# Kernel optimization log

Hardware: AMD Instinct MI355X
Metric: run time of the kernel (lower is better)

## Reference

```python
import jax, jax.numpy as jnp
import numpy as np

B, S, D = 2, 2048, 1024
NH, NKV = 16, 4
HD = D // NH
KVD = NKV * HD
NE, MM = 8, 4
INTER = MM * D // NE  # 512
ROPE_BASE = 10000.0
ALPHA, BETA, GATE, DT = 0.95, 0.3, 0.1, 0.1
MU_MIN, MU_MAX, VMAX = 0.5, 1.5, 3.0


def rms_norm(x):
    # torch F.rms_norm with eps=None -> finfo(dtype).eps, no learned weight
    return x * jax.lax.rsqrt(jnp.mean(x * x, axis=-1, keepdims=True) + jnp.finfo(x.dtype).eps)


def rope_tables(seq_len, dtype):
    inv_freq = 1.0 / ROPE_BASE ** (jnp.arange(0, HD, 2, dtype=jnp.float32) / HD)
    t = jnp.arange(seq_len, dtype=jnp.float32)
    freqs = jnp.outer(t, inv_freq)  # [S, HD/2]
    return jnp.cos(freqs).astype(dtype)[None, None], jnp.sin(freqs).astype(dtype)[None, None]


def apply_rotary(x, cos, sin):
    half = x.shape[-1] // 2
    x1, x2 = x[..., :half], x[..., half:]
    return jnp.concatenate((x1 * cos + x2 * sin, -x1 * sin + x2 * cos), axis=-1)


def attention(n, cq_w, ck_w, cv_w, proj_w, q_gain):
    q = jnp.einsum('bsd,od->bso', n, cq_w).reshape(B, S, NH, HD).transpose(0, 2, 1, 3)
    k = jnp.einsum('bsd,od->bso', n, ck_w).reshape(B, S, NKV, HD).transpose(0, 2, 1, 3)
    v = jnp.einsum('bsd,od->bso', n, cv_w).reshape(B, S, NKV, HD).transpose(0, 2, 1, 3)
    q, k = rms_norm(q), rms_norm(k)
    cos, sin = rope_tables(S, q.dtype)
    q, k = apply_rotary(q, cos, sin), apply_rotary(k, cos, sin)
    q = q * q_gain[None, :, None, None]
    rep = NH // NKV  # GQA: repeat kv heads
    k = jnp.repeat(k, rep, axis=1)
    v = jnp.repeat(v, rep, axis=1)
    scale = 1.0 / np.sqrt(HD).astype(np.float32)
    scores = jnp.einsum('bhqd,bhkd->bhqk', q, k) * scale
    causal = jnp.tril(jnp.ones((S, S), bool))
    scores = jnp.where(causal[None, None], scores, jnp.finfo(scores.dtype).min)
    probs = jax.nn.softmax(scores, axis=-1)
    y = jnp.einsum('bhqk,bhkd->bhqd', probs, v)
    y = y.transpose(0, 2, 1, 3).reshape(B, S, D)
    return jnp.einsum('bsd,od->bso', y, proj_w)


def moe(m, gate_up, down, eids):
    # faithful to TokenRoutedMLP: dense per-expert GEMM, masked accumulate
    flat = m.reshape(-1, D)
    fids = eids.reshape(-1)
    out = jnp.zeros_like(flat)
    for e in range(NE):
        gu = flat @ gate_up[e]                       # [T, 2*INTER]
        g, u = gu[:, :INTER], gu[:, INTER:]
        h = (jax.nn.silu(g) * u) @ down[e]           # [T, D]
        out = out + h * (fids == e)[:, None].astype(flat.dtype)
    return out.reshape(B, S, D)


def setup_inputs():
    key = jax.random.key(0)
    ks = jax.random.split(key, 10)
    w = lambda k, shape: jax.random.normal(k, shape, jnp.float32) * 0.02
    return {
        'x': jax.random.normal(ks[0], (B, S, D), jnp.float32),
        'x0': jax.random.normal(ks[1], (B, S, D), jnp.float32),
        'vel': jnp.zeros((B, S, D), jnp.float32),
        'resid_mix': jnp.stack((jnp.ones(D, jnp.float32), jnp.zeros(D, jnp.float32))),
        'attn_scale': jnp.ones(D, jnp.float32),
        'mlp_scale': jnp.ones(D, jnp.float32),
        'cq_w': w(ks[2], (D, D)),
        'ck_w': w(ks[3], (KVD, D)),
        'cv_w': w(ks[4], (KVD, D)),
        'proj_w': w(ks[5], (D, D)),
        'q_gain': jnp.ones(NH, jnp.float32),
        'mu': jnp.full((D,), 1.0, jnp.float32),
        'gate_up': w(ks[6], (NE, D, 2 * INTER)),
        'down': w(ks[7], (NE, INTER, D)),
        'eids': jax.random.randint(ks[8], (B, S), 0, NE),
    }


def reference(x, x0, vel, resid_mix, attn_scale, mlp_scale, cq_w, ck_w, cv_w, proj_w, q_gain, mu, gate_up, down, eids):
    x = resid_mix[0][None, None, :] * x + resid_mix[1][None, None, :] * x0
    n = rms_norm(x)
    x = x + attn_scale[None, None, :] * attention(n, cq_w, ck_w, cv_w, proj_w, q_gain)
    # PID dynamics
    mu_c = jnp.clip(mu, MU_MIN, MU_MAX)
    v_next = jnp.clip(ALPHA * vel - BETA * (x - mu_c[None, None, :]), -VMAX, VMAX)
    x = x + DT * GATE * v_next
    x = x + mlp_scale[None, None, :] * moe(rms_norm(x), gate_up, down, eids)
    return x, v_next
```

## Files before the change

### kernel.cpp

```cpp
#include <hip/hip_runtime.h>
#include <hip/hip_bf16.h>
#include <math.h>

#define NBATCH 2
#define NSEQ   2048
#define NDIM   1024
#define NHEAD  16
#define NKVH   4
#define HDIM   64
#define KVD    256
#define NEXP   8
#define NINTER 512
#define NTOK   (NBATCH*NSEQ)
#define QKVN   1536
#define MAXTILE 40
#define RMS_EPS 1.1920929e-07f
#define LN_10000 9.210340371976184f
#define QSCALE (0.125f * 1.44269504088896f)
#define DEFER_THR 11.5f
#define LOG2E 1.44269504088896f

typedef __attribute__((ext_vector_type(8))) short bf16x8;
typedef __attribute__((ext_vector_type(4))) short short4v;
typedef __attribute__((ext_vector_type(4))) float f32x4;

__device__ __forceinline__ short f2b(float f) {
  return __builtin_bit_cast(short, (__bf16)f);
}
__device__ __forceinline__ float b2f(short s) {
  unsigned u = ((unsigned)(unsigned short)s) << 16;
  return __builtin_bit_cast(float, u);
}
__device__ __forceinline__ float ex2(float x) {
  float r; asm("v_exp_f32 %0, %1" : "=v"(r) : "v"(x)); return r;
}
__device__ __forceinline__ void load_lds16(const short* g, short* l) {
  __builtin_amdgcn_global_load_lds((const __attribute__((address_space(1))) void*)g,
                                   (__attribute__((address_space(3))) void*)l, 16, 0, 0);
}

__device__ __forceinline__ float wred64(float v) {
#pragma unroll
  for (int m = 32; m >= 1; m >>= 1) v += __shfl_xor(v, m);
  return v;
}

__global__ __launch_bounds__(256) void k_w_prep(
    const float* __restrict__ cq, const float* __restrict__ ck,
    const float* __restrict__ cv, const float* __restrict__ pw,
    const float* __restrict__ gate_up,
    short* __restrict__ wqkv, short* __restrict__ wproj, short* __restrict__ wgu_t) {
  __shared__ short T[64*66];
  const int bid = blockIdx.x;
  const int t = threadIdx.x;
  if (bid < 2560) {
    const int row = bid;
    const int c = t * 4;
    const float* src; short* dst;
    if (row < 1024)      { src = cq + (size_t)row*NDIM;        dst = wqkv + (size_t)row*NDIM; }
    else if (row < 1280) { src = ck + (size_t)(row-1024)*NDIM; dst = wqkv + (size_t)row*NDIM; }
    else if (row < 1536) { src = cv + (size_t)(row-1280)*NDIM; dst = wqkv + (size_t)row*NDIM; }
    else                 { src = pw + (size_t)(row-1536)*NDIM; dst = wproj + (size_t)(row-1536)*NDIM; }
    float4 v = *(const float4*)(src + c);
    short4v o = {f2b(v.x), f2b(v.y), f2b(v.z), f2b(v.w)};
    *(short4v*)(dst + c) = o;
  } else {
    const int b2 = bid - 2560;
    const int kt = b2 & 15, nt = (b2 >> 4) & 15, e = b2 >> 8;
    const float* ie = gate_up + (size_t)e*1024*1024 + (size_t)(kt*64)*1024 + nt*64;
    short* we = wgu_t + (size_t)e*1024*1024;
    const int r = t >> 4, c = (t & 15) * 4;
#pragma unroll
    for (int p = 0; p < 4; ++p) {
      float4 v = *(const float4*)(ie + (size_t)(p*16 + r)*1024 + c);
      T[(p*16 + r)*66 + c + 0] = f2b(v.x);
      T[(p*16 + r)*66 + c + 1] = f2b(v.y);
      T[(p*16 + r)*66 + c + 2] = f2b(v.z);
      T[(p*16 + r)*66 + c + 3] = f2b(v.w);
    }
    __syncthreads();
#pragma unroll
    for (int p = 0; p < 4; ++p) {
      int rr = p*16 + r;
      int R = nt*64 + rr;
      int Rn = (R < 512) ? ((R & ~15)*2 + (R & 15))
                         : (((R - 512) & ~15)*2 + 16 + (R & 15));
      short4v o = {T[(c+0)*66 + rr], T[(c+1)*66 + rr], T[(c+2)*66 + rr], T[(c+3)*66 + rr]};
      *(short4v*)(we + (size_t)Rn*1024 + kt*64 + c) = o;
    }
  }
}

__global__ __launch_bounds__(256) void k_w_transpose(
    const float* __restrict__ in, short* __restrict__ outp, int KIN, int NIN) {
  __shared__ short T[64*66];
  const int kt = blockIdx.x, nt = blockIdx.y, e = blockIdx.z;
  const float* ie = in + (size_t)e*KIN*NIN + (size_t)(kt*64)*NIN + nt*64;
  short* oe = outp + (size_t)e*NIN*KIN + (size_t)(nt*64)*KIN + kt*64;
  const int t = threadIdx.x;
  const int r = t >> 4, c = (t & 15) * 4;
#pragma unroll
  for (int p = 0; p < 4; ++p) {
    float4 v = *(const float4*)(ie + (size_t)(p*16 + r)*NIN + c);
    T[(p*16 + r)*66 + c + 0] = f2b(v.x);
    T[(p*16 + r)*66 + c + 1] = f2b(v.y);
    T[(p*16 + r)*66 + c + 2] = f2b(v.z);
    T[(p*16 + r)*66 + c + 3] = f2b(v.w);
  }
  __syncthreads();
#pragma unroll
  for (int p = 0; p < 4; ++p) {
    int rr = p*16 + r;
    short4v o = {T[(c+0)*66 + rr], T[(c+1)*66 + rr], T[(c+2)*66 + rr], T[(c+3)*66 + rr]};
    *(short4v*)(oe + (size_t)rr*KIN + c) = o;
  }
}

__global__ __launch_bounds__(256) void k_resid_rms(
    const float* __restrict__ x, const float* __restrict__ x0,
    const float* __restrict__ rmix, short* __restrict__ xr, short* __restrict__ nrm) {
  const int row = blockIdx.x;
  const int t = threadIdx.x;
  const int d = t * 4;
  const size_t base = (size_t)row * NDIM + d;
  float4 a  = *(const float4*)(x  + base);
  float4 b  = *(const float4*)(x0 + base);
  float4 m0 = *(const float4*)(rmix + d);
  float4 m1 = *(const float4*)(rmix + NDIM + d);
  float4 r;
  r.x = m0.x*a.x + m1.x*b.x;
  r.y = m0.y*a.y + m1.y*b.y;
  r.z = m0.z*a.z + m1.z*b.z;
  r.w = m0.w*a.w + m1.w*b.w;
  float ss = r.x*r.x + r.y*r.y + r.z*r.z + r.w*r.w;
  ss = wred64(ss);
  __shared__ float wsum[4];
  if ((t & 63) == 0) wsum[t >> 6] = ss;
  __syncthreads();
  float tot = wsum[0] + wsum[1] + wsum[2] + wsum[3];
  float rms = rsqrtf(tot * (1.0f/NDIM) + RMS_EPS);
  short4v xo = {f2b(r.x), f2b(r.y), f2b(r.z), f2b(r.w)};
  short4v no = {f2b(r.x*rms), f2b(r.y*rms), f2b(r.z*rms), f2b(r.w*rms)};
  *(short4v*)(xr + base) = xo;
  *(short4v*)(nrm + base) = no;
}

template <int MODE>
__global__ __launch_bounds__(256) void k_gemm_mfma(
    const short* __restrict__ A, int lda,
    const short* __restrict__ Bw, int K, int N,
    short* __restrict__ Cb, float* __restrict__ Cf, int ldc,
    const int* __restrict__ rowmap, const int* __restrict__ tiletab,
    const int* __restrict__ meta, const float* __restrict__ mscale) {
  __shared__ short sA[2][128*32];
  __shared__ short sB[2][128*32];
  int row0, end = 0x7fffffff, e = 0;
  if (MODE == 0) {
    row0 = blockIdx.y * 128;
  } else {
    e = tiletab[2*blockIdx.y];
    if (e < 0) return;
    row0 = tiletab[2*blockIdx.y + 1];
    end = meta[1 + e];
  }
  const int t = threadIdx.x;
  const int w = t >> 6, l = t & 63;
  const int wr = (w >> 1) * 64, wc = (w & 1) * 64;
  const int lrow = l & 15, lk8 = (l >> 4) * 8;
  const int srow0 = w*16 + (l >> 2);
  const int scol = (l & 3) * 8;
  const short* Bp = Bw + (size_t)e * N * K + (size_t)(blockIdx.x * 128) * K;
  const short* gA0;
  const short* gA1;
  if (MODE == 1 || MODE == 3) {
    int s0 = row0 + srow0;      if (s0 >= NTOK) s0 = NTOK - 1;
    int s1 = row0 + 64 + srow0; if (s1 >= NTOK) s1 = NTOK - 1;
    gA0 = A + (size_t)rowmap[s0] * lda + scol;
    gA1 = A + (size_t)rowmap[s1] * lda + scol;
  } else {
    gA0 = A + (size_t)(row0 + srow0) * lda + scol;
    gA1 = A + (size_t)(row0 + 64 + srow0) * lda + scol;
  }
  const short* gB0 = Bp + (size_t)srow0 * K + scol;
  const short* gB1 = Bp + (size_t)(64 + srow0) * K + scol;
  const int lo0 = (w*16)*32;
  const int lo1 = (64 + w*16)*32;
  f32x4 acc[4][4];
#pragma unroll
  for (int m = 0; m < 4; ++m)
#pragma unroll
    for (int n = 0; n < 4; ++n) acc[m][n] = 0.f;
  load_lds16(gA0, sA[0] + lo0);
  load_lds16(gA1, sA[0] + lo1);
  load_lds16(gB0, sB[0] + lo0);
  load_lds16(gB1, sB[0] + lo1);
  gA0 += 32; gA1 += 32; gB0 += 32; gB1 += 32;
  int cur = 0;
  for (int k0 = 0; k0 < K; k0 += 32) {
    __syncthreads();
    if (k0 + 32 < K) {
      load_lds16(gA0, sA[cur^1] + lo0);
      load_lds16(gA1, sA[cur^1] + lo1);
      load_lds16(gB0, sB[cur^1] + lo0);
      load_lds16(gB1, sB[cur^1] + lo1);
      gA0 += 32; gA1 += 32; gB0 += 32; gB1 += 32;
    }
    bf16x8 af[4], bfr[4];
#pragma unroll
    for (int m = 0; m < 4; ++m)
      af[m] = *(const bf16x8*)&sA[cur][(wr + m*16 + lrow)*32 + lk8];
#pragma unroll
    for (int n = 0; n < 4; ++n)
      bfr[n] = *(const bf16x8*)&sB[cur][(wc + n*16 + lrow)*32 + lk8];
    __builtin_amdgcn_s_setprio(1);
#pragma unroll
    for (int m = 0; m < 4; ++m)
#pragma unroll
      for (int n = 0; n < 4; ++n)
        acc[m][n] = __builtin_amdgcn_mfma_f32_16x16x32_bf16(af[m], bfr[n], acc[m][n], 0, 0, 0);
    __builtin_amdgcn_s_setprio(0);
    cur ^= 1;
  }
  const int col0 = blockIdx.x * 128;
  if (MODE <= 1) {
#pragma unroll
    for (int m = 0; m < 4; ++m) {
#pragma unroll
      for (int r = 0; r < 4; ++r) {
        int rr = row0 + wr + m*16 + (l >> 4)*4 + r;
        if (rr < end) {
#pragma unroll
          for (int n = 0; n < 4; ++n)
            Cb[(size_t)rr * ldc + col0 + wc + n*16 + lrow] = f2b(acc[m][n][r]);
        }
      }
    }
  } else if (MODE == 2) {
#pragma unroll
    for (int m = 0; m < 4; ++m) {
#pragma unroll
      for (int r = 0; r < 4; ++r) {
        int slot = row0 + wr + m*16 + (l >> 4)*4 + r;
        if (slot < end) {
          int tok = rowmap[slot];
#pragma unroll
          for (int n = 0; n < 4; ++n) {
            int cc = col0 + wc + n*16 + lrow;
            Cf[(size_t)tok * ldc + cc] += mscale[cc] * acc[m][n][r];
          }
        }
      }
    }
  } else {
    const int fbBase = (col0 + wc) >> 5;
#pragma unroll
    for (int m = 0; m < 4; ++m) {
#pragma unroll
      for (int r = 0; r < 4; ++r) {
        int slot = row0 + wr + m*16 + (l >> 4)*4 + r;
        if (slot < end) {
#pragma unroll
          for (int p = 0; p < 2; ++p) {
            float gg = acc[m][2*p][r], uu = acc[m][2*p+1][r];
            float sg = 1.0f / (1.0f + ex2(-LOG2E * gg));
            Cb[(size_t)slot * NINTER + (fbBase + p)*16 + lrow] = f2b(gg * sg * uu);
          }
        }
      }
    }
  }
}

__global__ __launch_bounds__(256) void k_qk_norm_rope(
    short* __restrict__ qkv, const float* __restrict__ q_gain, short* __restrict__ vbT) {
  __shared__ short T[64*72];
  const int row = blockIdx.x;
  const int t = threadIdx.x;
  const int w = t >> 6, lane = t & 63;
  const int s = row & (NSEQ - 1);
  const int fi = lane & 31;
  const float fr = (float)s * expf(-(float)fi * (LN_10000 / 32.0f));
  const float co = cosf(fr), si = sinf(fr);
#pragma unroll
  for (int h = w; h < NHEAD; h += 4) {
    short* p = qkv + (size_t)row*QKVN + h*HDIM + lane;
    float v = b2f(*p);
    float ssum = wred64(v*v);
    float rr = rsqrtf(ssum * (1.0f/HDIM) + RMS_EPS);
    float vn = v * rr;
    float partner = __shfl_xor(vn, 32);
    float o = (lane < 32) ? (vn*co + partner*si) : (vn*co - partner*si);
    *p = f2b(o * q_gain[h] * QSCALE);
  }
  if (w < NKVH) {
    short* p = qkv + (size_t)row*QKVN + 1024 + w*HDIM + lane;
    float v = b2f(*p);
    float ssum = wred64(v*v);
    float rr = rsqrtf(ssum * (1.0f/HDIM) + RMS_EPS);
    float vn = v * rr;
    float partner = __shfl_xor(vn, 32);
    float o = (lane < 32) ? (vn*co + partner*si) : (vn*co - partner*si);
    *p = f2b(o);
  }
  if (row < 256) {
    const int st = row & 31, kh = (row >> 5) & 3, b = row >> 7;
#pragma unroll
    for (int i = 0; i < 2; ++i) {
      int c = t + i*256;
      int sV = c >> 3, d0 = (c & 7) * 8;
      bf16x8 v = *(const bf16x8*)(qkv + (size_t)(b*NSEQ + st*64 + sV)*QKVN + 1280 + kh*HDIM + d0);
#pragma unroll
      for (int j = 0; j < 8; ++j) T[(d0 + j)*72 + sV] = v[j];
    }
    __syncthreads();
#pragma unroll
    for (int i = 0; i < 2; ++i) {
      int c = t + i*256;
      int d = c >> 3, s0 = (c & 7) * 8;
      *(bf16x8*)(vbT + (size_t)((b*NKVH + kh)*HDIM + d)*NSEQ + st*64 + s0) = *(bf16x8*)&T[d*72 + s0];
    }
  }
}

__global__ __launch_bounds__(256) void k_attn_mfma(
    const short* __restrict__ qkv, const short* __restrict__ vbT, short* __restrict__ y) {
  __shared__ short Ks[2][64*72];
  __shared__ short Vt[2][64*72];
  __shared__ short Ps[64*72];
  const int t = threadIdx.x;
  const int l = t & 63, w = t >> 6;
  const int lrow = l & 15, g = l >> 4, lk8 = g * 8;
  const int bid = blockIdx.x;
  int qt = bid & 15;
  const int h = (bid >> 4) & 15, b = bid >> 8;
  if (b & 1) qt = 15 - qt;
  const int kh = h >> 2;
  bf16x8 qf[2][2];
#pragma unroll
  for (int qra = 0; qra < 2; ++qra) {
    int qrow_g = b*NSEQ + qt*128 + qra*64 + w*16 + lrow;
#pragma unroll
    for (int hf = 0; hf < 2; ++hf)
      qf[qra][hf] = *(const bf16x8*)(qkv + (size_t)qrow_g*QKVN + h*HDIM + hf*32 + lk8);
  }
  const int r0a = t >> 3;
  const int d0a = (t & 7) * 8;
  const short* kgbase = qkv + 1024 + (size_t)kh*HDIM;
  const short* vgbase = vbT + (size_t)((b*NKVH + kh)*HDIM)*NSEQ;
  bf16x8 kr0, kr1, vr0, vr1;
#define LOADKV(KT) do { \
    kr0 = *(const bf16x8*)(kgbase + (size_t)(b*NSEQ + (KT)*64 + r0a)*QKVN + d0a); \
    kr1 = *(const bf16x8*)(kgbase + (size_t)(b*NSEQ + (KT)*64 + r0a + 32)*QKVN + d0a); \
    vr0 = *(const bf16x8*)(vgbase + (size_t)r0a*NSEQ + (KT)*64 + d0a); \
    vr1 = *(const bf16x8*)(vgbase + (size_t)(r0a + 32)*NSEQ + (KT)*64 + d0a); \
  } while (0)
  float m_i[2] = {-INFINITY, -INFINITY};
  float l_i[2] = {0.f, 0.f};
  f32x4 O[2][4];
#pragma unroll
  for (int qra = 0; qra < 2; ++qra)
#pragma unroll
    for (int db = 0; db < 4; ++db) O[qra][db] = 0.f;
  const int ktmax = 2*qt + 1;
  LOADKV(0);
  for (int kt = 0; kt <= ktmax; ++kt) {
    const int buf = kt & 1;
    *(bf16x8*)&Ks[buf][r0a*72 + d0a] = kr0;
    *(bf16x8*)&Ks[buf][(r0a + 32)*72 + d0a] = kr1;
    *(bf16x8*)&Vt[buf][r0a*72 + d0a] = vr0;
    *(bf16x8*)&Vt[buf][(r0a + 32)*72 + d0a] = vr1;
    __syncthreads();
    if (kt < ktmax) LOADKV(kt + 1);
    bf16x8 kf[4][2];
#pragma unroll
    for (int nb = 0; nb < 4; ++nb) {
      kf[nb][0] = *(const bf16x8*)&Ks[buf][(nb*16 + lrow)*72 + lk8];
      kf[nb][1] = *(const bf16x8*)&Ks[buf][(nb*16 + lrow)*72 + 32 + lk8];
    }
    const int qra0 = (kt == ktmax) ? 1 : 0;
    bf16x8 pf[2][2];
#pragma unroll
    for (int qra = 0; qra < 2; ++qra) {
      if (qra >= qra0) {
        f32x4 sc[4];
#pragma unroll
        for (int nb = 0; nb < 4; ++nb) sc[nb] = 0.f;
        __builtin_amdgcn_s_setprio(1);
#pragma unroll
        for (int nb = 0; nb < 4; ++nb) {
          sc[nb] = __builtin_amdgcn_mfma_f32_16x16x32_bf16(kf[nb][0], qf[qra][0], sc[nb], 0, 0, 0);
          sc[nb] = __builtin_amdgcn_mfma_f32_16x16x32_bf16(kf[nb][1], qf[qra][1], sc[nb], 0, 0, 0);
        }
        __builtin_amdgcn_s_setprio(0);
        if (kt >= 2*qt) {
          int qg = qt*128 + qra*64 + w*16 + lrow;
#pragma unroll
          for (int nb = 0; nb < 4; ++nb)
#pragma unroll
            for (int r = 0; r < 4; ++r)
              if (kt*64 + nb*16 + g*4 + r > qg) sc[nb][r] = -INFINITY;
        }
        float rm = sc[0][0];
#pragma unroll
        for (int nb = 0; nb < 4; ++nb)
#pragma unroll
          for (int r = 0; r < 4; ++r) rm = fmaxf(rm, sc[nb][r]);
        rm = fmaxf(rm, __shfl_xor(rm, 16));
        rm = fmaxf(rm, __shfl_xor(rm, 32));
        if (!__all(rm <= m_i[qra] + DEFER_THR)) {
          float mn = fmaxf(m_i[qra], rm);
          float fac = ex2(m_i[qra] - mn);
          l_i[qra] *= fac;
          m_i[qra] = mn;
#pragma unroll
          for (int r = 0; r < 4; ++r) {
            float ff = __shfl(fac, g*4 + r);
#pragma unroll
            for (int db = 0; db < 4; ++db) O[qra][db][r] *= ff;
          }
        }
        float rs = 0.f;
#pragma unroll
        for (int nb = 0; nb < 4; ++nb) {
#pragma unroll
          for (int r = 0; r < 4; ++r) {
            float p = ex2(sc[nb][r] - m_i[qra]);
            sc[nb][r] = p;
            rs += p;
          }
        }
        rs += __shfl_xor(rs, 16);
        rs += __shfl_xor(rs, 32);
        l_i[qra] += rs;
        short* prow = &Ps[(w*16 + lrow)*72];
#pragma unroll
        for (int nb = 0; nb < 4; ++nb) {
          short4v pk = {f2b(sc[nb][0]), f2b(sc[nb][1]), f2b(sc[nb][2]), f2b(sc[nb][3])};
          *(short4v*)(prow + nb*16 + g*4) = pk;
        }
        pf[qra][0] = *(const bf16x8*)&Ps[(w*16 + lrow)*72 + lk8];
        pf[qra][1] = *(const bf16x8*)&Ps[(w*16 + lrow)*72 + 32 + lk8];
      }
    }
    __builtin_amdgcn_s_setprio(1);
#pragma unroll
    for (int db = 0; db < 4; ++db) {
      bf16x8 vf0 = *(const bf16x8*)&Vt[buf][(db*16 + lrow)*72 + lk8];
      bf16x8 vf1 = *(const bf16x8*)&Vt[buf][(db*16 + lrow)*72 + 32 + lk8];
      if (qra0 == 0) {
        O[0][db] = __builtin_amdgcn_mfma_f32_16x16x32_bf16(pf[0][0], vf0, O[0][db], 0, 0, 0);
        O[0][db] = __builtin_amdgcn_mfma_f32_16x16x32_bf16(pf[0][1], vf1, O[0][db], 0, 0, 0);
      }
      O[1][db] = __builtin_amdgcn_mfma_f32_16x16x32_bf16(pf[1][0], vf0, O[1][db], 0, 0, 0);
      O[1][db] = __builtin_amdgcn_mfma_f32_16x16x32_bf16(pf[1][1], vf1, O[1][db], 0, 0, 0);
    }
    __builtin_amdgcn_s_setprio(0);
  }
#undef LOADKV
#pragma unroll
  for (int qra = 0; qra < 2; ++qra) {
    float linv = 1.0f / l_i[qra];
#pragma unroll
    for (int r = 0; r < 4; ++r) {
      float inv = __shfl(linv, g*4 + r);
      int rowo = b*NSEQ + qt*128 + qra*64 + w*16 + g*4 + r;
#pragma unroll
      for (int db = 0; db < 4; ++db)
        y[(size_t)rowo*NDIM + h*HDIM + db*16 + lrow] = f2b(O[qra][db][r] * inv);
    }
  }
}

__global__ __launch_bounds__(256) void k_fuse_vel(
    const short* __restrict__ xr, const short* __restrict__ aout,
    const float* __restrict__ vel, const float* __restrict__ ascale,
    const float* __restrict__ mu, float* __restrict__ out, short* __restrict__ mbuf,
    const int* __restrict__ eids, int* __restrict__ rowmap,
    int* __restrict__ tiletab, int* __restrict__ meta) {
  const int row = blockIdx.x;
  const int t = threadIdx.x;
  const int d = t * 4;
  const size_t base = (size_t)row * NDIM + d;
  short4v a4 = *(const short4v*)(xr + base);
  short4v o4 = *(const short4v*)(aout + base);
  float4 vv = *(const float4*)(vel + base);
  float4 as = *(const float4*)(ascale + d);
  float4 mu4 = *(const float4*)(mu + d);
  float xs[4], vns[4];
  const float asl[4] = {as.x, as.y, as.z, as.w};
  const float mul[4] = {mu4.x, mu4.y, mu4.z, mu4.w};
  const float vvl[4] = {vv.x, vv.y, vv.z, vv.w};
#pragma unroll
  for (int i = 0; i < 4; ++i) {
    float x1 = b2f(a4[i]) + asl[i] * b2f(o4[i]);
    float muc = fminf(fmaxf(mul[i], 0.5f), 1.5f);
    float vn = fminf(fmaxf(0.95f*vvl[i] - 0.3f*(x1 - muc), -3.f), 3.f);
    xs[i] = x1 + 0.01f*vn;
    vns[i] = vn;
  }
  float4 x2 = {xs[0], xs[1], xs[2], xs[3]};
  float4 vnq = {vns[0], vns[1], vns[2], vns[3]};
  *(float4*)(out + base) = x2;
  *(float4*)(out + (size_t)NTOK*NDIM + base) = vnq;
  float ss = xs[0]*xs[0] + xs[1]*xs[1] + xs[2]*xs[2] + xs[3]*xs[3];
  ss = wred64(ss);
  __shared__ float wsum[4];
  if ((t & 63) == 0) wsum[t >> 6] = ss;
  __syncthreads();
  float tot = wsum[0] + wsum[1] + wsum[2] + wsum[3];
  float rms = rsqrtf(tot * (1.0f/NDIM) + RMS_EPS);
  short4v m4 = {f2b(xs[0]*rms), f2b(xs[1]*rms), f2b(xs[2]*rms), f2b(xs[3]*rms)};
  *(short4v*)(mbuf + base) = m4;
  if (blockIdx.x == 0) {
    __shared__ int cnt[NEXP];
    __shared__ int ctr[NEXP];
    if (t < NEXP) cnt[t] = 0;
    __syncthreads();
    for (int i = t; i < NTOK; i += 256) atomicAdd(&cnt[eids[i]], 1);
    __syncthreads();
    if (t == 0) {
      int off = 0, tile = 0;
      for (int e = 0; e < NEXP; ++e) {
        ctr[e] = off;
        int nt_e = (cnt[e] + 127) >> 7;
        for (int j = 0; j < nt_e; ++j) { tiletab[2*tile] = e; tiletab[2*tile+1] = off + j*128; ++tile; }
        off += cnt[e];
        meta[1 + e] = off;
      }
      meta[0] = tile;
      for (int j = tile; j < MAXTILE; ++j) { tiletab[2*j] = -1; tiletab[2*j+1] = 0; }
    }
    __syncthreads();
    for (int i = t; i < NTOK; i += 256) {
      int e = eids[i];
      int slot = atomicAdd(&ctr[e], 1);
      rowmap[slot] = i;
    }
  }
}

extern "C" void kernel_launch(void* const* d_in, const int* in_sizes, int n_in,
                              void* d_out, int out_size, void* d_ws, size_t ws_size,
                              hipStream_t stream) {
  const float* x      = (const float*)d_in[0];
  const float* x0     = (const float*)d_in[1];
  const float* vel    = (const float*)d_in[2];
  const float* rmix   = (const float*)d_in[3];
  const float* ascale = (const float*)d_in[4];
  const float* mscale = (const float*)d_in[5];
  const float* cq_w   = (const float*)d_in[6];
  const float* ck_w   = (const float*)d_in[7];
  const float* cv_w   = (const float*)d_in[8];
  const float* proj_w = (const float*)d_in[9];
  const float* q_gain = (const float*)d_in[10];
  const float* mu     = (const float*)d_in[11];
  const float* gate_up= (const float*)d_in[12];
  const float* down   = (const float*)d_in[13];
  const int*   eids   = (const int*)d_in[14];
  float* out = (float*)d_out;
  char* base = (char*)d_ws;

  const size_t MB = 1024*1024;
  short* wqkv  = (short*)base;
  short* wproj = (short*)(base + 3*MB);
  int*   rowmap  = (int*)(base + 5*MB);
  int*   tiletab = rowmap + NTOK;
  int*   meta    = tiletab + 2*MAXTILE;
  short* wgu_t = (short*)(base + 6*MB);
  short* xr    = (short*)(base + 22*MB);
  short* hbuf  = xr;
  short* nbuf  = (short*)(base + 30*MB);
  short* ybuf  = nbuf;
  short* mbuf  = nbuf;
  short* wdn_t = nbuf;
  short* qkv   = (short*)(base + 38*MB);
  short* aout  = qkv;
  short* vbT   = (short*)(base + 50*MB);

  k_w_prep<<<4608, 256, 0, stream>>>(cq_w, ck_w, cv_w, proj_w, gate_up, wqkv, wproj, wgu_t);
  k_resid_rms<<<NTOK, 256, 0, stream>>>(x, x0, rmix, xr, nbuf);
  k_gemm_mfma<0><<<dim3(QKVN/128, NTOK/128), 256, 0, stream>>>(
      nbuf, NDIM, wqkv, NDIM, QKVN, qkv, nullptr, QKVN, nullptr, nullptr, nullptr, nullptr);
  k_qk_norm_rope<<<NTOK, 256, 0, stream>>>(qkv, q_gain, vbT);
  k_attn_mfma<<<NBATCH*NHEAD*(NSEQ/128), 256, 0, stream>>>(qkv, vbT, ybuf);
  k_gemm_mfma<0><<<dim3(NDIM/128, NTOK/128), 256, 0, stream>>>(
      ybuf, NDIM, wproj, NDIM, NDIM, aout, nullptr, NDIM, nullptr, nullptr, nullptr, nullptr);
  k_fuse_vel<<<NTOK, 256, 0, stream>>>(xr, aout, vel, ascale, mu, out, mbuf,
                                       eids, rowmap, tiletab, meta);
  k_gemm_mfma<3><<<dim3(1024/128, MAXTILE), 256, 0, stream>>>(
      mbuf, NDIM, wgu_t, NDIM, 1024, hbuf, nullptr, NINTER, rowmap, tiletab, meta, nullptr);
  k_w_transpose<<<dim3(8, 16, 8), 256, 0, stream>>>(down, wdn_t, 512, 1024);
  k_gemm_mfma<2><<<dim3(NDIM/128, MAXTILE), 256, 0, stream>>>(
      hbuf, NINTER, wdn_t, NINTER, NDIM, nullptr, out, NDIM, rowmap, tiletab, meta, mscale);
}
```

Baseline: 217.7 us.

## Keep attention probabilities in registers by permuting V tile layout in LDS

```diff
diff --git a/kernel.cpp b/kernel.cpp
--- a/kernel.cpp
+++ b/kernel.cpp
@@ -326,7 +326,6 @@
     const short* __restrict__ qkv, const short* __restrict__ vbT, short* __restrict__ y) {
   __shared__ short Ks[2][64*72];
   __shared__ short Vt[2][64*72];
-  __shared__ short Ps[64*72];
   const int t = threadIdx.x;
   const int l = t & 63, w = t >> 6;
   const int lrow = l & 15, g = l >> 4, lk8 = g * 8;
@@ -345,6 +344,8 @@
   }
   const int r0a = t >> 3;
   const int d0a = (t & 7) * 8;
+  const int mseg = t & 7;
+  const int vb0 = (mseg >> 2)*32 + (mseg & 1)*16 + ((mseg >> 1) & 1)*4;
   const short* kgbase = qkv + 1024 + (size_t)kh*HDIM;
   const short* vgbase = vbT + (size_t)((b*NKVH + kh)*HDIM)*NSEQ;
   bf16x8 kr0, kr1, vr0, vr1;
@@ -367,8 +368,14 @@
     const int buf = kt & 1;
     *(bf16x8*)&Ks[buf][r0a*72 + d0a] = kr0;
     *(bf16x8*)&Ks[buf][(r0a + 32)*72 + d0a] = kr1;
-    *(bf16x8*)&Vt[buf][r0a*72 + d0a] = vr0;
-    *(bf16x8*)&Vt[buf][(r0a + 32)*72 + d0a] = vr1;
+    {
+      short4v* v0p = (short4v*)&vr0;
+      short4v* v1p = (short4v*)&vr1;
+      *(short4v*)&Vt[buf][r0a*72 + vb0]            = v0p[0];
+      *(short4v*)&Vt[buf][r0a*72 + vb0 + 8]        = v0p[1];
+      *(short4v*)&Vt[buf][(r0a + 32)*72 + vb0]     = v1p[0];
+      *(short4v*)&Vt[buf][(r0a + 32)*72 + vb0 + 8] = v1p[1];
+    }
     __syncthreads();
     if (kt < ktmax) LOADKV(kt + 1);
     bf16x8 kf[4][2];
@@ -432,14 +439,21 @@
         rs += __shfl_xor(rs, 16);
         rs += __shfl_xor(rs, 32);
         l_i[qra] += rs;
-        short* prow = &Ps[(w*16 + lrow)*72];
+        unsigned pk[4][2];
 #pragma unroll
         for (int nb = 0; nb < 4; ++nb) {
-          short4v pk = {f2b(sc[nb][0]), f2b(sc[nb][1]), f2b(sc[nb][2]), f2b(sc[nb][3])};
-          *(short4v*)(prow + nb*16 + g*4) = pk;
-        }
-        pf[qra][0] = *(const bf16x8*)&Ps[(w*16 + lrow)*72 + lk8];
-        pf[qra][1] = *(const bf16x8*)&Ps[(w*16 + lrow)*72 + 32 + lk8];
+          asm("v_cvt_pk_bf16_f32 %0, %1, %2" : "=v"(pk[nb][0]) : "v"(sc[nb][0]), "v"(sc[nb][1]));
+          asm("v_cvt_pk_bf16_f32 %0, %1, %2" : "=v"(pk[nb][1]) : "v"(sc[nb][2]), "v"(sc[nb][3]));
+        }
+#pragma unroll
+        for (int H = 0; H < 2; ++H) {
+          union { unsigned u[4]; bf16x8 v; } P;
+          P.u[0] = pk[2*H][0];
+          P.u[1] = pk[2*H][1];
+          P.u[2] = pk[2*H+1][0];
+          P.u[3] = pk[2*H+1][1];
+          pf[qra][H] = P.v;
+        }
       }
     }
     __builtin_amdgcn_s_setprio(1);
```

Result: no change. 214.8 us, median of 2 (-1.3%).
